# Performance work log

Hardware: AMD Instinct MI355X
Metric: run time of the kernel (lower is better)

## Reference

```python
import jax, jax.numpy as jnp
import numpy as np

N_HEADS, N_KV, HEAD_DIM, D_MODEL, T_MAX = 16, 4, 64, 1024, 2048
GROUPS = N_HEADS // N_KV
EPS = 1e-6


def _rms_norm(x, w):
    # RMSNorm over last dim (head_dim), computed in fp32 like the torch module
    xf = x.astype(jnp.float32)
    r = jax.lax.rsqrt(jnp.mean(xf * xf, axis=-1, keepdims=True) + EPS)
    return (xf * r).astype(x.dtype) * w


def _apply_rope(x, cos, sin):
    # x: (B, H, T, D); cos/sin: (T_max, D/2)
    T = x.shape[2]
    c = cos[:T][None, None]  # (1,1,T,D/2)
    s = sin[:T][None, None]
    x1, x2 = jnp.split(x, 2, axis=-1)
    return jnp.concatenate([x1 * c - x2 * s, x2 * c + x1 * s], axis=-1)


def setup_inputs() -> dict:
    key = jax.random.key(0)
    ks = jax.random.split(key, 8)
    B, T = 2, 2048
    x = jax.random.normal(ks[0], (B, T, D_MODEL), dtype=jnp.float32)
    # realistic RoPE tables
    theta = 10000.0
    inv_freq = 1.0 / (theta ** (np.arange(0, HEAD_DIM, 2, dtype=np.float32) / HEAD_DIM))
    t = np.arange(T_MAX, dtype=np.float32)
    freqs = np.outer(t, inv_freq)  # (T_max, D/2)
    cos = jnp.asarray(np.cos(freqs))
    sin = jnp.asarray(np.sin(freqs))
    sd = 0.02
    wq = jax.random.normal(ks[1], (N_HEADS * HEAD_DIM, D_MODEL), dtype=jnp.float32) * sd
    wk = jax.random.normal(ks[2], (N_KV * HEAD_DIM, D_MODEL), dtype=jnp.float32) * sd
    wv = jax.random.normal(ks[3], (N_KV * HEAD_DIM, D_MODEL), dtype=jnp.float32) * sd
    wo = jax.random.normal(ks[4], (D_MODEL, N_HEADS * HEAD_DIM), dtype=jnp.float32) * sd
    qn_w = jnp.ones((HEAD_DIM,), dtype=jnp.float32)
    kn_w = jnp.ones((HEAD_DIM,), dtype=jnp.float32)
    return {"x": x, "cos": cos, "sin": sin, "wq": wq, "wk": wk, "wv": wv,
            "wo": wo, "qn_w": qn_w, "kn_w": kn_w}


def reference(x, cos, sin, wq, wk, wv, wo, qn_w, kn_w):
    B, T, _ = x.shape
    scale = HEAD_DIM ** -0.5
    # projections (torch Linear: y = x @ W.T)
    q = (x @ wq.T).reshape(B, T, N_HEADS, HEAD_DIM).transpose(0, 2, 1, 3)
    k = (x @ wk.T).reshape(B, T, N_KV, HEAD_DIM).transpose(0, 2, 1, 3)
    v = (x @ wv.T).reshape(B, T, N_KV, HEAD_DIM).transpose(0, 2, 1, 3)
    # qk RMSNorm
    q = _rms_norm(q, qn_w)
    k = _rms_norm(k, kn_w)
    # RoPE
    q = _apply_rope(q, cos, sin)
    k = _apply_rope(k, cos, sin)
    # GQA expansion: query head h uses kv head h // GROUPS
    k = jnp.repeat(k, GROUPS, axis=1)  # (B, H, T, D)
    v = jnp.repeat(v, GROUPS, axis=1)
    # causal SDPA
    scores = jnp.einsum('bhqd,bhkd->bhqk', q, k) * scale
    causal = jnp.tril(jnp.ones((T, T), dtype=bool))
    scores = jnp.where(causal, scores, jnp.finfo(scores.dtype).min)
    p = jax.nn.softmax(scores, axis=-1)
    out = jnp.einsum('bhqk,bhkd->bhqd', p, v)
    out = out.transpose(0, 2, 1, 3).reshape(B, T, N_HEADS * HEAD_DIM)
    return out @ wo.T
```

## Files before the change

### kernel.cpp

```cpp
#include <hip/hip_runtime.h>


typedef __bf16 bf16;
typedef __attribute__((ext_vector_type(4))) __bf16 bf16x4;
typedef __attribute__((ext_vector_type(8))) __bf16 bf16x8;
typedef __attribute__((ext_vector_type(4))) float f32x4;

#define MFMA(a, b, c) __builtin_amdgcn_mfma_f32_16x16x32_bf16((a), (b), (c), 0, 0, 0)
#define GLOAD_LDS16(g, l)                                        \
  __builtin_amdgcn_global_load_lds(                              \
      (const __attribute__((address_space(1))) void*)(g),        \
      (__attribute__((address_space(3))) void*)(l), 16, 0, 0)

__device__ __forceinline__ bool is_bf16_input(const void* cosRaw) {
  return ((const unsigned short*)cosRaw)[0] == 0x3F80;
}
__device__ __forceinline__ float rdval(const void* p, int idx, bool isbf) {
  return isbf ? (float)((const bf16*)p)[idx] : ((const float*)p)[idx];
}

__device__ __forceinline__ void stage_rows(const void* src, size_t rowbase,
                                           int ko, int srow, int csrc,
                                           int lane, bf16* ls, bool isbf) {
  if (isbf) {
    GLOAD_LDS16(&((const bf16*)src)[(rowbase + srow) * 1024 + ko + csrc * 8], ls);
  } else {
    const float* fp = &((const float*)src)[(rowbase + srow) * 1024 + ko + csrc * 8];
    float4 f0 = *(const float4*)fp;
    float4 f1 = *(const float4*)(fp + 4);
    bf16x8 o;
    o[0] = (bf16)f0.x; o[1] = (bf16)f0.y; o[2] = (bf16)f0.z; o[3] = (bf16)f0.w;
    o[4] = (bf16)f1.x; o[5] = (bf16)f1.y; o[6] = (bf16)f1.z; o[7] = (bf16)f1.w;
    *(bf16x8*)&ls[lane * 8] = o;
  }
}

__global__ __launch_bounds__(256) void convert_kernel(
    const void* __restrict__ x, const void* __restrict__ wq,
    const void* __restrict__ wk, const void* __restrict__ wv,
    bf16* __restrict__ dx, bf16* __restrict__ dw,
    const void* __restrict__ cosraw) {
  const bool isbf = is_bf16_input(cosraw);
  const int c = (int)blockIdx.x * 256 + (int)threadIdx.x;
  const void* src;
  int off;
  bf16* dst;
  int dc;
  if (c < 524288)      { src = x;  off = c;          dst = dx; dc = c; }
  else if (c < 655360) { src = wq; off = c - 524288; dst = dw; dc = c - 524288; }
  else if (c < 688128) { src = wk; off = c - 655360; dst = dw; dc = c - 524288; }
  else                 { src = wv; off = c - 688128; dst = dw; dc = c - 524288; }
  bf16x8 o;
  if (isbf) {
    o = ((const bf16x8*)src)[off];
  } else {
    const float4* fp = (const float4*)src + (size_t)off * 2;
    float4 f0 = fp[0];
    float4 f1 = fp[1];
    o[0] = (bf16)f0.x; o[1] = (bf16)f0.y; o[2] = (bf16)f0.z; o[3] = (bf16)f0.w;
    o[4] = (bf16)f1.x; o[5] = (bf16)f1.y; o[6] = (bf16)f1.z; o[7] = (bf16)f1.w;
  }
  ((bf16x8*)dst)[dc] = o;
}

__global__ __launch_bounds__(256, 3) void proj_kernel(
    const bf16* __restrict__ xb, const bf16* __restrict__ wqb,
    const bf16* __restrict__ wkb, const bf16* __restrict__ wvb,
    bf16* __restrict__ qp, bf16* __restrict__ kp, bf16* __restrict__ vt,
    const void* __restrict__ cosraw, const void* __restrict__ sinraw,
    const void* __restrict__ qnraw, const void* __restrict__ knraw) {
  __shared__ bf16 As[128 * 64];
  __shared__ bf16 Bs[64 * 64];

  const int idx = (int)blockIdx.x;
  const int xcd = idx & 7;
  const int jj = idx >> 3;
  const int mb = (jj & 3) * 8 + xcd;
  const int nb = jj >> 2;
  const int n0 = nb * 64;
  const int m0 = mb * 128;

  const int tid = threadIdx.x;
  const int wave = tid >> 6;
  const int lane = tid & 63;
  const int q16 = lane & 15;
  const int quad = lane >> 4;
  const int srow = lane >> 3;
  const int csrc = (lane & 7) ^ srow;
  const int x7 = q16 & 7;

  const bf16* wsrc;
  int nr0;
  if (nb < 16)      { wsrc = wqb; nr0 = n0; }
  else if (nb < 20) { wsrc = wkb; nr0 = n0 - 1024; }
  else              { wsrc = wvb; nr0 = n0 - 1280; }

  f32x4 acc[2][4];
#pragma unroll
  for (int mf = 0; mf < 2; ++mf)
#pragma unroll
    for (int nt = 0; nt < 4; ++nt) acc[mf][nt] = (f32x4){0.f, 0.f, 0.f, 0.f};

  for (int kt = 0; kt < 16; ++kt) {
    const int ko = kt * 64;
#pragma unroll
    for (int i = 0; i < 4; ++i) {
      int rb = wave * 32 + i * 8;
      GLOAD_LDS16(&xb[(size_t)(m0 + rb + srow) * 1024 + ko + csrc * 8],
                  &As[rb * 64]);
    }
#pragma unroll
    for (int i = 0; i < 2; ++i) {
      int rb = wave * 16 + i * 8;
      GLOAD_LDS16(&wsrc[(size_t)(nr0 + rb + srow) * 1024 + ko + csrc * 8],
                  &Bs[rb * 64]);
    }
    __syncthreads();

    bf16x8 a[2][2], bfr[4][2];
#pragma unroll
    for (int mf = 0; mf < 2; ++mf) {
      const bf16* rp = &As[(wave * 32 + mf * 16 + q16) * 64];
      a[mf][0] = *(const bf16x8*)&rp[(quad ^ x7) * 8];
      a[mf][1] = *(const bf16x8*)&rp[((quad + 4) ^ x7) * 8];
    }
#pragma unroll
    for (int nt = 0; nt < 4; ++nt) {
      const bf16* rp = &Bs[(nt * 16 + q16) * 64];
      bfr[nt][0] = *(const bf16x8*)&rp[(quad ^ x7) * 8];
      bfr[nt][1] = *(const bf16x8*)&rp[((quad + 4) ^ x7) * 8];
    }
#pragma unroll
    for (int nt = 0; nt < 4; ++nt)
#pragma unroll
      for (int mf = 0; mf < 2; ++mf) {
        acc[mf][nt] = MFMA(a[mf][0], bfr[nt][0], acc[mf][nt]);
        acc[mf][nt] = MFMA(a[mf][1], bfr[nt][1], acc[mf][nt]);
      }
    __syncthreads();
  }

  if (nb < 20) {
    const bool isbf = is_bf16_input(cosraw);
    const void* nwp = (nb < 16) ? qnraw : knraw;
    const float osc = (nb < 16) ? 0.125f : 1.0f;
    float wd[4];
#pragma unroll
    for (int nt = 0; nt < 4; ++nt) wd[nt] = rdval(nwp, nt * 16 + q16, isbf);

#pragma unroll
    for (int mf = 0; mf < 2; ++mf) {
#pragma unroll
      for (int r = 0; r < 4; ++r) {
        float p = acc[mf][0][r] * acc[mf][0][r] + acc[mf][1][r] * acc[mf][1][r] +
                  acc[mf][2][r] * acc[mf][2][r] + acc[mf][3][r] * acc[mf][3][r];
#pragma unroll
        for (int off = 8; off >= 1; off >>= 1) p += __shfl_xor(p, off);
        float rms = rsqrtf(p * (1.0f / 64.0f) + 1e-6f);

        int row = m0 + wave * 32 + mf * 16 + quad * 4 + r;
        int t = row & 2047;
        float c0 = rdval(cosraw, t * 32 + q16, isbf);
        float c1 = rdval(cosraw, t * 32 + 16 + q16, isbf);
        float s0 = rdval(sinraw, t * 32 + q16, isbf);
        float s1 = rdval(sinraw, t * 32 + 16 + q16, isbf);

        float v0 = acc[mf][0][r] * rms * wd[0];
        float v1 = acc[mf][1][r] * rms * wd[1];
        float v2 = acc[mf][2][r] * rms * wd[2];
        float v3 = acc[mf][3][r] * rms * wd[3];

        bf16* op = (nb < 16) ? &qp[(size_t)row * 1024 + nb * 64]
                             : &kp[(size_t)row * 256 + (nb - 16) * 64];
        op[0 * 16 + q16] = (bf16)((v0 * c0 - v2 * s0) * osc);
        op[1 * 16 + q16] = (bf16)((v1 * c1 - v3 * s1) * osc);
        op[2 * 16 + q16] = (bf16)((v2 * c0 + v0 * s0) * osc);
        op[3 * 16 + q16] = (bf16)((v3 * c1 + v1 * s1) * osc);
      }
    }
  } else {
    const int vh = nb - 20;
    const int b = m0 >> 11;
    const int tbase = m0 & 2047;
#pragma unroll
    for (int mf = 0; mf < 2; ++mf)
#pragma unroll
      for (int nt = 0; nt < 4; ++nt)
#pragma unroll
        for (int r = 0; r < 4; ++r)
          As[(wave * 32 + mf * 16 + quad * 4 + r) * 64 + nt * 16 + q16] =
              (bf16)acc[mf][nt][r];
    __syncthreads();
#pragma unroll
    for (int rep = 0; rep < 4; ++rep) {
      int c = tid + 256 * rep;
      int d = c >> 4;
      int t8 = (c & 15) * 8;
      bf16x8 pk;
#pragma unroll
      for (int j = 0; j < 8; ++j) pk[j] = As[(t8 + j) * 64 + d];
      *(bf16x8*)&vt[(((size_t)(b * 4 + vh)) * 64 + d) * 2048 + tbase + t8] = pk;
    }
  }
}

__global__ __launch_bounds__(256, 4) void flash_kernel(
    const bf16* __restrict__ qp, const bf16* __restrict__ kp,
    const bf16* __restrict__ vt, bf16* __restrict__ attn) {
  const int qblk = blockIdx.z ? 31 - (int)blockIdx.x : (int)blockIdx.x;
  const int h = blockIdx.y;
  const int b = blockIdx.z;
  const int kvh = h >> 2;
  const int tid = threadIdx.x;
  const int wave = tid >> 6;
  const int lane = tid & 63;
  const int q16 = lane & 15;
  const int quad = lane >> 4;
  const int r7 = q16 & 7;
  const int t0 = qblk * 64 + wave * 16;

  __shared__ bf16 Ks[2][64 * 64];
  __shared__ bf16 Vs[2][64 * 64];
  __shared__ bf16 Pl[4][16 * 32];

  const bf16* qrow = qp + (((size_t)(b * 2048 + t0 + q16)) * 16 + h) * 64;
  bf16x8 qa0 = *(const bf16x8*)(qrow + quad * 8);
  bf16x8 qa1 = *(const bf16x8*)(qrow + 32 + quad * 8);

  bf16x8 ones;
#pragma unroll
  for (int j = 0; j < 8; ++j) ones[j] = (bf16)1.0f;

  f32x4 O[4], l4;
#pragma unroll
  for (int nt = 0; nt < 4; ++nt) O[nt] = (f32x4){0.f, 0.f, 0.f, 0.f};
  l4 = (f32x4){0.f, 0.f, 0.f, 0.f};

  const int ntile = qblk + 1;

  bf16x8 kr[2], vr[2];
  const int cr = tid * 2;
  const int krow = cr >> 3;
  const size_t kgbase = (((size_t)(b * 2048) + krow) * 4 + kvh) * 64;
  const size_t vgbase = ((size_t)(b * 4 + kvh) * 64 + krow) * 2048;

  auto gload = [&](int tk) {
#pragma unroll
    for (int rep = 0; rep < 2; ++rep) {
      int ch = (cr + rep) & 7;
      kr[rep] = *(const bf16x8*)&kp[kgbase + (size_t)(tk * 64) * 256 + ch * 8];
      vr[rep] = *(const bf16x8*)&vt[vgbase + tk * 64 + ch * 8];
    }
  };
  auto swrite = [&](int bb) {
#pragma unroll
    for (int rep = 0; rep < 2; ++rep) {
      int ch = (cr + rep) & 7;
      int pos = (ch ^ (krow & 7)) * 8;
      *(bf16x8*)&Ks[bb][krow * 64 + pos] = kr[rep];
      *(bf16x8*)&Vs[bb][krow * 64 + pos] = vr[rep];
    }
  };

  gload(0);

  for (int t = 0; t < ntile; ++t) {
    const int bb = t & 1;
    const int kbase = t * 64;
    swrite(bb);
    __syncthreads();
    if (t + 1 < ntile) gload(t + 1);

    f32x4 s[4];
#pragma unroll
    for (int kt = 0; kt < 4; ++kt) {
      const bf16* kr0 = &Ks[bb][(kt * 16 + q16) * 64];
      bf16x8 kb0 = *(const bf16x8*)&kr0[(quad ^ r7) * 8];
      bf16x8 kb1 = *(const bf16x8*)&kr0[((quad + 4) ^ r7) * 8];
      f32x4 z = (f32x4){0.f, 0.f, 0.f, 0.f};
      z = MFMA(kb0, qa0, z);
      z = MFMA(kb1, qa1, z);
      s[kt] = z;
    }

    if (kbase + 63 > t0) {
      const int q = t0 + q16;
#pragma unroll
      for (int kt = 0; kt < 4; ++kt) {
        int jt = kbase + kt * 16 + quad * 4;
#pragma unroll
        for (int r = 0; r < 4; ++r)
          if (jt + r > q) s[kt][r] = -1e30f;
      }
    }

#pragma unroll
    for (int kt = 0; kt < 4; ++kt)
#pragma unroll
      for (int r = 0; r < 4; ++r) s[kt][r] = __expf(s[kt][r] - 9.0f);

#pragma unroll
    for (int kh = 0; kh < 2; ++kh) {
#pragma unroll
      for (int ct = 0; ct < 2; ++ct) {
        const int kt = kh * 2 + ct;
        bf16x4 pk;
#pragma unroll
        for (int r = 0; r < 4; ++r) pk[r] = (bf16)s[kt][r];
        *(bf16x4*)&Pl[wave][q16 * 32 + ((ct * 4 + quad) ^ (q16 & 6)) * 4] = pk;
      }
      bf16x8 pa = *(const bf16x8*)&Pl[wave][q16 * 32 + ((quad * 2) ^ (q16 & 6)) * 4];
#pragma unroll
      for (int nt = 0; nt < 4; ++nt) {
        const bf16* vr0 = &Vs[bb][(nt * 16 + q16) * 64];
        bf16x8 vb = *(const bf16x8*)&vr0[((kh * 4 + quad) ^ r7) * 8];
        O[nt] = MFMA(pa, vb, O[nt]);
      }
      l4 = MFMA(pa, ones, l4);
    }
  }

  float inv[4];
#pragma unroll
  for (int r = 0; r < 4; ++r) inv[r] = 1.0f / l4[r];
#pragma unroll
  for (int nt = 0; nt < 4; ++nt)
#pragma unroll
    for (int r = 0; r < 4; ++r) {
      size_t o = (((size_t)(b * 2048 + t0 + quad * 4 + r)) * 16 + h) * 64 +
                 nt * 16 + q16;
      attn[o] = (bf16)(O[nt][r] * inv[r]);
    }
}

__global__ __launch_bounds__(256, 2) void gemm_o_kernel(
    const bf16* __restrict__ A, const void* __restrict__ Wraw,
    void* __restrict__ C, const void* __restrict__ cosraw) {
  __shared__ bf16 As[128 * 64];
  __shared__ bf16 Bs[64 * 64];

  const int idx = (int)blockIdx.x;
  const int xcd = idx & 7;
  const int jj = idx >> 3;
  const int mb = (jj & 3) * 8 + xcd;
  const int nb = jj >> 2;
  const int n0 = nb * 64;
  const int m0 = mb * 128;

  const int tid = threadIdx.x;
  const int wave = tid >> 6;
  const int lane = tid & 63;
  const int q16 = lane & 15;
  const int quad = lane >> 4;
  const int srow = lane >> 3;
  const int csrc = (lane & 7) ^ srow;
  const int x7 = q16 & 7;
  const bool isbf = is_bf16_input(cosraw);

  f32x4 acc[2][4];
#pragma unroll
  for (int mf = 0; mf < 2; ++mf)
#pragma unroll
    for (int nt = 0; nt < 4; ++nt) acc[mf][nt] = (f32x4){0.f, 0.f, 0.f, 0.f};

  for (int kt = 0; kt < 16; ++kt) {
    const int ko = kt * 64;
#pragma unroll
    for (int i = 0; i < 4; ++i) {
      int rb = wave * 32 + i * 8;
      GLOAD_LDS16(&A[(size_t)(m0 + rb + srow) * 1024 + ko + csrc * 8],
                  &As[rb * 64]);
    }
#pragma unroll
    for (int i = 0; i < 2; ++i) {
      int rb = wave * 16 + i * 8;
      stage_rows(Wraw, (size_t)(n0 + rb), ko, srow, csrc, lane, &Bs[rb * 64], isbf);
    }
    __syncthreads();

    bf16x8 a[2][2], bfr[4][2];
#pragma unroll
    for (int mf = 0; mf < 2; ++mf) {
      const bf16* rp = &As[(wave * 32 + mf * 16 + q16) * 64];
      a[mf][0] = *(const bf16x8*)&rp[(quad ^ x7) * 8];
      a[mf][1] = *(const bf16x8*)&rp[((quad + 4) ^ x7) * 8];
    }
#pragma unroll
    for (int nt = 0; nt < 4; ++nt) {
      const bf16* rp = &Bs[(nt * 16 + q16) * 64];
      bfr[nt][0] = *(const bf16x8*)&rp[(quad ^ x7) * 8];
      bfr[nt][1] = *(const bf16x8*)&rp[((quad + 4) ^ x7) * 8];
    }
#pragma unroll
    for (int nt = 0; nt < 4; ++nt)
#pragma unroll
      for (int mf = 0; mf < 2; ++mf) {
        acc[mf][nt] = MFMA(a[mf][0], bfr[nt][0], acc[mf][nt]);
        acc[mf][nt] = MFMA(a[mf][1], bfr[nt][1], acc[mf][nt]);
      }
    __syncthreads();
  }

#pragma unroll
  for (int mf = 0; mf < 2; ++mf)
#pragma unroll
    for (int nt = 0; nt < 4; ++nt)
#pragma unroll
      for (int r = 0; r < 4; ++r) {
        size_t idx2 = (size_t)(m0 + wave * 32 + mf * 16 + quad * 4 + r) * 1024 +
                      n0 + nt * 16 + q16;
        if (isbf) ((bf16*)C)[idx2] = (bf16)acc[mf][nt][r];
        else      ((float*)C)[idx2] = acc[mf][nt][r];
      }
}

extern "C" void kernel_launch(void* const* d_in, const int* in_sizes, int n_in,
                              void* d_out, int out_size, void* d_ws, size_t ws_size,
                              hipStream_t stream) {
  bf16* qp = (bf16*)d_ws;
  bf16* kp = qp + (size_t)4096 * 1024;
  bf16* vt = kp + (size_t)4096 * 256;
  bf16* at = vt + (size_t)4096 * 256;

  bf16* xb = at;
  bf16* wqb = (bf16*)d_out;
  bf16* wkb = wqb + (size_t)1048576;
  bf16* wvb = wkb + (size_t)262144;

  convert_kernel<<<2816, 256, 0, stream>>>(
      d_in[0], d_in[3], d_in[4], d_in[5], xb, wqb, d_in[1]);

  proj_kernel<<<768, 256, 0, stream>>>(
      xb, wqb, wkb, wvb, qp, kp, vt,
      d_in[1], d_in[2], d_in[7], d_in[8]);

  flash_kernel<<<dim3(32, 16, 2), 256, 0, stream>>>(qp, kp, vt, at);

  gemm_o_kernel<<<512, 256, 0, stream>>>(at, d_in[6], d_out, d_in[1]);
}
```

Before: 163.5 us.

## Pre-convert wo to bf16 and shrink output GEMM tiles for more blocks

Measured after the change: 155.7 us, median of 2. 4.7% less time.

```diff
diff --git a/kernel.cpp b/kernel.cpp
--- a/kernel.cpp
+++ b/kernel.cpp
@@ -19,27 +19,11 @@
   return isbf ? (float)((const bf16*)p)[idx] : ((const float*)p)[idx];
 }
 
-__device__ __forceinline__ void stage_rows(const void* src, size_t rowbase,
-                                           int ko, int srow, int csrc,
-                                           int lane, bf16* ls, bool isbf) {
-  if (isbf) {
-    GLOAD_LDS16(&((const bf16*)src)[(rowbase + srow) * 1024 + ko + csrc * 8], ls);
-  } else {
-    const float* fp = &((const float*)src)[(rowbase + srow) * 1024 + ko + csrc * 8];
-    float4 f0 = *(const float4*)fp;
-    float4 f1 = *(const float4*)(fp + 4);
-    bf16x8 o;
-    o[0] = (bf16)f0.x; o[1] = (bf16)f0.y; o[2] = (bf16)f0.z; o[3] = (bf16)f0.w;
-    o[4] = (bf16)f1.x; o[5] = (bf16)f1.y; o[6] = (bf16)f1.z; o[7] = (bf16)f1.w;
-    *(bf16x8*)&ls[lane * 8] = o;
-  }
-}
-
 __global__ __launch_bounds__(256) void convert_kernel(
     const void* __restrict__ x, const void* __restrict__ wq,
     const void* __restrict__ wk, const void* __restrict__ wv,
-    bf16* __restrict__ dx, bf16* __restrict__ dw,
-    const void* __restrict__ cosraw) {
+    const void* __restrict__ wo, bf16* __restrict__ dx,
+    bf16* __restrict__ dw, const void* __restrict__ cosraw) {
   const bool isbf = is_bf16_input(cosraw);
   const int c = (int)blockIdx.x * 256 + (int)threadIdx.x;
   const void* src;
@@ -49,7 +33,8 @@
   if (c < 524288)      { src = x;  off = c;          dst = dx; dc = c; }
   else if (c < 655360) { src = wq; off = c - 524288; dst = dw; dc = c - 524288; }
   else if (c < 688128) { src = wk; off = c - 655360; dst = dw; dc = c - 524288; }
-  else                 { src = wv; off = c - 688128; dst = dw; dc = c - 524288; }
+  else if (c < 720896) { src = wv; off = c - 688128; dst = dw; dc = c - 524288; }
+  else                 { src = wo; off = c - 720896; dst = dw; dc = c - 524288; }
   bf16x8 o;
   if (isbf) {
     o = ((const bf16x8*)src)[off];
@@ -333,19 +318,19 @@
     }
 }
 
-__global__ __launch_bounds__(256, 2) void gemm_o_kernel(
-    const bf16* __restrict__ A, const void* __restrict__ Wraw,
+__global__ __launch_bounds__(256, 6) void gemm_o_kernel(
+    const bf16* __restrict__ A, const bf16* __restrict__ W,
     void* __restrict__ C, const void* __restrict__ cosraw) {
-  __shared__ bf16 As[128 * 64];
+  __shared__ bf16 As[64 * 64];
   __shared__ bf16 Bs[64 * 64];
 
   const int idx = (int)blockIdx.x;
   const int xcd = idx & 7;
   const int jj = idx >> 3;
-  const int mb = (jj & 3) * 8 + xcd;
-  const int nb = jj >> 2;
+  const int mb = (jj & 7) * 8 + xcd;
+  const int nb = jj >> 3;
   const int n0 = nb * 64;
-  const int m0 = mb * 128;
+  const int m0 = mb * 64;
 
   const int tid = threadIdx.x;
   const int wave = tid >> 6;
@@ -354,36 +339,31 @@
   const int quad = lane >> 4;
   const int srow = lane >> 3;
   const int csrc = (lane & 7) ^ srow;
+  const int wm = wave * 16;
   const int x7 = q16 & 7;
   const bool isbf = is_bf16_input(cosraw);
 
-  f32x4 acc[2][4];
-#pragma unroll
-  for (int mf = 0; mf < 2; ++mf)
-#pragma unroll
-    for (int nt = 0; nt < 4; ++nt) acc[mf][nt] = (f32x4){0.f, 0.f, 0.f, 0.f};
+  f32x4 acc[4];
+#pragma unroll
+  for (int nt = 0; nt < 4; ++nt) acc[nt] = (f32x4){0.f, 0.f, 0.f, 0.f};
 
   for (int kt = 0; kt < 16; ++kt) {
     const int ko = kt * 64;
 #pragma unroll
-    for (int i = 0; i < 4; ++i) {
-      int rb = wave * 32 + i * 8;
+    for (int i = 0; i < 2; ++i) {
+      int rb = wave * 16 + i * 8;
       GLOAD_LDS16(&A[(size_t)(m0 + rb + srow) * 1024 + ko + csrc * 8],
                   &As[rb * 64]);
-    }
-#pragma unroll
-    for (int i = 0; i < 2; ++i) {
-      int rb = wave * 16 + i * 8;
-      stage_rows(Wraw, (size_t)(n0 + rb), ko, srow, csrc, lane, &Bs[rb * 64], isbf);
-    }
-    __syncthreads();
-
-    bf16x8 a[2][2], bfr[4][2];
-#pragma unroll
-    for (int mf = 0; mf < 2; ++mf) {
-      const bf16* rp = &As[(wave * 32 + mf * 16 + q16) * 64];
-      a[mf][0] = *(const bf16x8*)&rp[(quad ^ x7) * 8];
-      a[mf][1] = *(const bf16x8*)&rp[((quad + 4) ^ x7) * 8];
+      GLOAD_LDS16(&W[(size_t)(n0 + rb + srow) * 1024 + ko + csrc * 8],
+                  &Bs[rb * 64]);
+    }
+    __syncthreads();
+
+    bf16x8 a0, a1, bfr[4][2];
+    {
+      const bf16* rp = &As[(wm + q16) * 64];
+      a0 = *(const bf16x8*)&rp[(quad ^ x7) * 8];
+      a1 = *(const bf16x8*)&rp[((quad + 4) ^ x7) * 8];
     }
 #pragma unroll
     for (int nt = 0; nt < 4; ++nt) {
@@ -392,43 +372,40 @@
       bfr[nt][1] = *(const bf16x8*)&rp[((quad + 4) ^ x7) * 8];
     }
 #pragma unroll
-    for (int nt = 0; nt < 4; ++nt)
-#pragma unroll
-      for (int mf = 0; mf < 2; ++mf) {
-        acc[mf][nt] = MFMA(a[mf][0], bfr[nt][0], acc[mf][nt]);
-        acc[mf][nt] = MFMA(a[mf][1], bfr[nt][1], acc[mf][nt]);
-      }
+    for (int nt = 0; nt < 4; ++nt) {
+      acc[nt] = MFMA(a0, bfr[nt][0], acc[nt]);
+      acc[nt] = MFMA(a1, bfr[nt][1], acc[nt]);
+    }
     __syncthreads();
   }
 
 #pragma unroll
-  for (int mf = 0; mf < 2; ++mf)
-#pragma unroll
-    for (int nt = 0; nt < 4; ++nt)
-#pragma unroll
-      for (int r = 0; r < 4; ++r) {
-        size_t idx2 = (size_t)(m0 + wave * 32 + mf * 16 + quad * 4 + r) * 1024 +
-                      n0 + nt * 16 + q16;
-        if (isbf) ((bf16*)C)[idx2] = (bf16)acc[mf][nt][r];
-        else      ((float*)C)[idx2] = acc[mf][nt][r];
-      }
+  for (int nt = 0; nt < 4; ++nt)
+#pragma unroll
+    for (int r = 0; r < 4; ++r) {
+      size_t idx2 = (size_t)(m0 + wm + quad * 4 + r) * 1024 + n0 + nt * 16 + q16;
+      if (isbf) ((bf16*)C)[idx2] = (bf16)acc[nt][r];
+      else      ((float*)C)[idx2] = acc[nt][r];
+    }
 }
 
 extern "C" void kernel_launch(void* const* d_in, const int* in_sizes, int n_in,
                               void* d_out, int out_size, void* d_ws, size_t ws_size,
                               hipStream_t stream) {
   bf16* qp = (bf16*)d_ws;
-  bf16* kp = qp + (size_t)4096 * 1024;
-  bf16* vt = kp + (size_t)4096 * 256;
-  bf16* at = vt + (size_t)4096 * 256;
-
-  bf16* xb = at;
-  bf16* wqb = (bf16*)d_out;
-  bf16* wkb = wqb + (size_t)1048576;
-  bf16* wvb = wkb + (size_t)262144;
-
-  convert_kernel<<<2816, 256, 0, stream>>>(
-      d_in[0], d_in[3], d_in[4], d_in[5], xb, wqb, d_in[1]);
+  bf16* kp = qp + (size_t)4194304;
+  bf16* vt = kp + (size_t)1048576;
+  bf16* at = vt + (size_t)1048576;
+  bf16* xb = at + (size_t)4194304;
+  bf16* dw = xb + (size_t)4194304;
+
+  bf16* wqb = dw;
+  bf16* wkb = dw + (size_t)1048576;
+  bf16* wvb = dw + (size_t)1310720;
+  bf16* wob = dw + (size_t)1572864;
+
+  convert_kernel<<<3328, 256, 0, stream>>>(
+      d_in[0], d_in[3], d_in[4], d_in[5], d_in[6], xb, dw, d_in[1]);
 
   proj_kernel<<<768, 256, 0, stream>>>(
       xb, wqb, wkb, wvb, qp, kp, vt,
@@ -436,5 +413,5 @@
 
   flash_kernel<<<dim3(32, 16, 2), 256, 0, stream>>>(qp, kp, vt, at);
 
-  gemm_o_kernel<<<512, 256, 0, stream>>>(at, d_in[6], d_out, d_in[1]);
-}
+  gemm_o_kernel<<<1024, 256, 0, stream>>>(at, wob, d_out, d_in[1]);
+}
```
